# Optimization experiments

Measured on AMD Instinct MI355X. Metric: run time of the kernel, lower is better.

The kernel has to match this reference:

```python
import jax, jax.numpy as jnp
import numpy as np

N = 6720      # 16 graphs * 420 nodes
E = 33600     # 16 graphs * 2100 edges (5 per node)
DIN = 2048
H1, C1 = 2, 1024   # conv1: heads=2, out=1024 -> concat 2048
H2, C2 = 1, 64     # conv2: heads=1, out=64
ED = 64            # edge_dim
NODES_PER_GRAPH = 420


def _lin(k, fi, fo):
    return jax.random.normal(k, (fi, fo), jnp.float32) / np.sqrt(fi).astype(np.float32)


def setup_inputs() -> dict:
    key = jax.random.key(0)
    ks = jax.random.split(key, 24)
    d = {}
    d["x"] = jax.random.normal(ks[0], (N, DIN), jnp.float32)
    d["edge_index"] = jax.random.randint(ks[1], (2, E), 0, N)
    # tiled learned edge_features param (torch.rand init), one 2100xED block per graph
    ef = jax.random.uniform(ks[2], (5 * NODES_PER_GRAPH, ED), jnp.float32)
    d["edge_attr"] = jnp.tile(ef, (N // NODES_PER_GRAPH, 1))
    HC1 = H1 * C1
    d["q1_w"] = _lin(ks[3], DIN, HC1); d["q1_b"] = jax.random.normal(ks[4], (HC1,)) * 0.01
    d["k1_w"] = _lin(ks[5], DIN, HC1); d["k1_b"] = jax.random.normal(ks[6], (HC1,)) * 0.01
    d["v1_w"] = _lin(ks[7], DIN, HC1); d["v1_b"] = jax.random.normal(ks[8], (HC1,)) * 0.01
    d["e1_w"] = _lin(ks[9], ED, HC1)                      # lin_edge has no bias in PyG
    d["s1_w"] = _lin(ks[10], DIN, HC1); d["s1_b"] = jax.random.normal(ks[11], (HC1,)) * 0.01
    HC2 = H2 * C2
    d["q2_w"] = _lin(ks[12], HC1, HC2); d["q2_b"] = jax.random.normal(ks[13], (HC2,)) * 0.01
    d["k2_w"] = _lin(ks[14], HC1, HC2); d["k2_b"] = jax.random.normal(ks[15], (HC2,)) * 0.01
    d["v2_w"] = _lin(ks[16], HC1, HC2); d["v2_b"] = jax.random.normal(ks[17], (HC2,)) * 0.01
    d["e2_w"] = _lin(ks[18], ED, HC2)
    d["s2_w"] = _lin(ks[19], HC1, HC2); d["s2_b"] = jax.random.normal(ks[20], (HC2,)) * 0.01
    return d


def _transformer_conv(x, src, dst, edge_attr, qw, qb, kw, kb, vw, vb, ew, sw, sb, H, C):
    """PyG TransformerConv (concat=True, beta=False, root_weight=True)."""
    n = x.shape[0]
    q = (x @ qw + qb).reshape(n, H, C)
    k = (x @ kw + kb).reshape(n, H, C)
    v = (x @ vw + vb).reshape(n, H, C)
    e = (edge_attr @ ew).reshape(-1, H, C)         # [E,H,C]
    kj = k[src] + e                                # gather source keys + edge emb
    alpha = jnp.sum(q[dst] * kj, axis=-1) / np.sqrt(C).astype(np.float32)  # [E,H]
    # scatter-softmax over incoming edges of each target node
    amax = jax.ops.segment_max(alpha, dst, num_segments=n)   # [N,H]
    ex = jnp.exp(alpha - amax[dst])
    denom = jax.ops.segment_sum(ex, dst, num_segments=n)
    attn = ex / (denom[dst] + 1e-16)               # [E,H]
    msg = (v[src] + e) * attn[..., None]           # [E,H,C]
    out = jax.ops.segment_sum(msg, dst, num_segments=n).reshape(n, H * C)
    return out + x @ sw + sb                       # root/skip connection


def reference(x, edge_index, edge_attr,
              q1_w, q1_b, k1_w, k1_b, v1_w, v1_b, e1_w, s1_w, s1_b,
              q2_w, q2_b, k2_w, k2_b, v2_w, v2_b, e2_w, s2_w, s2_b):
    src, dst = edge_index[0], edge_index[1]
    h = jax.nn.relu(_transformer_conv(x, src, dst, edge_attr,
                                      q1_w, q1_b, k1_w, k1_b, v1_w, v1_b,
                                      e1_w, s1_w, s1_b, H1, C1))
    h = jax.nn.relu(_transformer_conv(h, src, dst, edge_attr,
                                      q2_w, q2_b, k2_w, k2_b, v2_w, v2_b,
                                      e2_w, s2_w, s2_b, H2, C2))
    return h.reshape(-1, NODES_PER_GRAPH * 64)     # forward returns here (fc layers are dead code)
```

## Files before the change

### kernel.cpp

```cpp
#include <hip/hip_runtime.h>
#include <hip/hip_bf16.h>
#include <cstdint>
#include <cstddef>

#define NN    6720
#define MPAD  6912
#define NE    33600
#define KDIM  2048
#define HC1   2048
#define EAP   2100

typedef __attribute__((ext_vector_type(8))) short bhalf8;
typedef __attribute__((ext_vector_type(4))) short bhalf4;
typedef __attribute__((ext_vector_type(4))) float fx4;

__device__ __forceinline__ float bf2f(short s) {
    union { unsigned int u; float f; } c;
    c.u = ((unsigned int)(unsigned short)s) << 16;
    return c.f;
}

__device__ __forceinline__ void gload16(const __hip_bfloat16* g, void* lds)
{
    __builtin_amdgcn_global_load_lds(
        (const __attribute__((address_space(1))) unsigned int*)g,
        (__attribute__((address_space(3))) unsigned int*)lds,
        16, 0, 0);
}

#define CFENCE asm volatile("" ::: "memory")

__global__ __launch_bounds__(256, 2) void gemm256x128_fused(
    const __hip_bfloat16* __restrict__ A,
    const __hip_bfloat16* __restrict__ Bt,
    const float* __restrict__ bcat,
    __hip_bfloat16* __restrict__ oq,
    __hip_bfloat16* __restrict__ ok,
    __hip_bfloat16* __restrict__ ov,
    float* __restrict__ oh)
{
    __shared__ alignas(16) char Lds[73728];

    const int tid  = threadIdx.x;
    const int w    = tid >> 6;
    const int lane = tid & 63;
    const int wm = w >> 1, wn = w & 1;
    const int sug = ((lane & 3) ^ ((lane >> 3) & 3)) << 3;
    const int rds = (((lane >> 4) ^ (((lane & 15) >> 1) & 3)) << 4);

#define STAGE(T)                                                          \
    { const int s_ = (T) % 3; const int k0_ = (T) * 32;                   \
      char* ab_ = Lds + s_ * 16384 + w * 4096;                            \
      char* bb_ = Lds + 49152 + s_ * 8192 + w * 2048;                     \
      gload16(Ag0 + k0_, ab_);                                            \
      gload16(Ag0 + k0_ + 16 * KDIM, ab_ + 1024);                         \
      gload16(Ag0 + k0_ + 32 * KDIM, ab_ + 2048);                         \
      gload16(Ag0 + k0_ + 48 * KDIM, ab_ + 3072);                         \
      gload16(Bg0 + k0_, bb_);                                            \
      gload16(Bg0 + k0_ + 16 * KDIM, bb_ + 1024); }

#define TILE(T, VM, DOSTAGE)                                              \
    { if (DOSTAGE) { STAGE((T) + 2); }                                    \
      asm volatile("s_waitcnt vmcnt(" VM ")" ::: "memory");               \
      __builtin_amdgcn_s_barrier(); CFENCE;                               \
      const int s_ = (T) % 3;                                             \
      const char* ap_ = Lds + s_ * 16384;                                 \
      const char* bp_ = Lds + 49152 + s_ * 8192;                          \
      bhalf8 af_[8], bf_[4];                                              \
      _Pragma("unroll")                                                   \
      for (int nj = 0; nj < 4; ++nj)                                      \
          bf_[nj] = *(const bhalf8*)(bp_ + (wn * 64 + nj * 16 + (lane & 15)) * 64 + rds); \
      _Pragma("unroll")                                                   \
      for (int mi = 0; mi < 8; ++mi)                                      \
          af_[mi] = *(const bhalf8*)(ap_ + (wm * 128 + mi * 16 + (lane & 15)) * 64 + rds); \
      __builtin_amdgcn_s_setprio(1);                                      \
      _Pragma("unroll")                                                   \
      for (int mi = 0; mi < 8; ++mi)                                      \
          _Pragma("unroll")                                               \
          for (int nj = 0; nj < 4; ++nj)                                  \
              acc[mi][nj] = __builtin_amdgcn_mfma_f32_16x16x32_bf16(      \
                  af_[mi], bf_[nj], acc[mi][nj], 0, 0, 0);                \
      __builtin_amdgcn_s_setprio(0); CFENCE;                              \
      __builtin_amdgcn_s_barrier(); CFENCE; }

    for (int vt = blockIdx.x; vt < 1728; vt += 512) {
        if (vt != (int)blockIdx.x) {
            asm volatile("s_waitcnt vmcnt(0)" ::: "memory");
            __builtin_amdgcn_s_barrier();
            CFENCE;
        }
        const int i0 = vt >> 3;
        const int bx = (vt & 7) * 8 + (i0 & 7);
        const int by = i0 >> 3;
        const int rowA = by * 256;
        const int rowB = bx * 128;
        const __hip_bfloat16* Ag0 = A  + (size_t)(rowA + w * 64 + (lane >> 2)) * KDIM + sug;
        const __hip_bfloat16* Bg0 = Bt + (size_t)(rowB + w * 32 + (lane >> 2)) * KDIM + sug;

        fx4 acc[8][4] = {};

        STAGE(0); STAGE(1);
        for (int t = 0; t < (KDIM / 32) - 2; ++t) {
            TILE(t, "12", 1);
        }
        TILE((KDIM / 32) - 2, "6", 0);
        TILE((KDIM / 32) - 1, "0", 0);

        const int gcol = rowB + wn * 64;
        const int seg  = gcol >> 11;
        const int lcol = gcol & 2047;
        float bv[4];
        #pragma unroll
        for (int nj = 0; nj < 4; ++nj) bv[nj] = bcat[gcol + nj * 16 + (lane & 15)];
        char* scr = Lds + w * 8704;
        const int growA = rowA + wm * 128;

        #pragma unroll
        for (int c = 0; c < 4; ++c) {
            #pragma unroll
            for (int m2 = 0; m2 < 2; ++m2) {
                const int mi = c * 2 + m2;
                #pragma unroll
                for (int nj = 0; nj < 4; ++nj) {
                    const int cl = nj * 16 + (lane & 15);
                    #pragma unroll
                    for (int i2 = 0; i2 < 4; ++i2) {
                        const int rl = m2 * 16 + ((lane >> 4) << 2) + i2;
                        *(float*)(scr + rl * 272 + cl * 4) = acc[mi][nj][i2] + bv[nj];
                    }
                }
            }
            asm volatile("s_waitcnt lgkmcnt(0)" ::: "memory");
            CFENCE;
            const int rrow = (lane >> 4);
            const int u    = lane & 15;
            if (seg < 3) {
                __hip_bfloat16* dst = (seg == 0) ? oq : (seg == 1) ? ok : ov;
                #pragma unroll
                for (int p = 0; p < 8; ++p) {
                    const int row = p * 4 + rrow;
                    const float4 f = *(const float4*)(scr + row * 272 + u * 16);
                    bhalf4 tb;
                    tb[0] = (short)__bfloat16_as_ushort(__float2bfloat16(f.x));
                    tb[1] = (short)__bfloat16_as_ushort(__float2bfloat16(f.y));
                    tb[2] = (short)__bfloat16_as_ushort(__float2bfloat16(f.z));
                    tb[3] = (short)__bfloat16_as_ushort(__float2bfloat16(f.w));
                    *(bhalf4*)&dst[(size_t)(growA + c * 32 + row) * 2048 + lcol + u * 4] = tb;
                }
            } else {
                #pragma unroll
                for (int p = 0; p < 8; ++p) {
                    const int row = p * 4 + rrow;
                    const float4 f = *(const float4*)(scr + row * 272 + u * 16);
                    *(float4*)&oh[(size_t)(growA + c * 32 + row) * 2048 + lcol + u * 4] = f;
                }
            }
            asm volatile("s_waitcnt lgkmcnt(0)" ::: "memory");
            CFENCE;
        }
    }
#undef TILE
#undef STAGE
}

__global__ __launch_bounds__(256) void gemm_bf16(
    const __hip_bfloat16* __restrict__ A,
    const __hip_bfloat16* __restrict__ Bt,
    const float* __restrict__ bias,
    float* __restrict__ C,
    __hip_bfloat16* __restrict__ Cb,
    int M, int N, int K, int flags)
{
    __shared__ alignas(16) __hip_bfloat16 Asm[128 * 64];
    __shared__ alignas(16) __hip_bfloat16 Bsm[128 * 64];
    const int tid  = threadIdx.x;
    const int w    = tid >> 6;
    const int lane = tid & 63;
    const int wr = w >> 1, wc = w & 1;
    const int rowA = blockIdx.y * 128;
    const int rowB = blockIdx.x * 128;
    const int klen = K / gridDim.z;
    const int kbeg = blockIdx.z * klen;

    const int srow = w * 32 + (lane >> 3);
    const int ug8  = ((lane & 7) ^ (lane >> 3)) << 3;
    const __hip_bfloat16* Ag = A  + (size_t)(rowA + srow) * K + ug8;
    const __hip_bfloat16* Bg = Bt + (size_t)(rowB + srow) * K + ug8;
    char* AsBase = (char*)Asm + w * 4096;
    char* BsBase = (char*)Bsm + w * 4096;

    fx4 acc[4][4] = {};

    const int fra = wr * 64 + (lane & 15);
    const int frb = wc * 64 + (lane & 15);
    const int kb  = (lane >> 4) << 4;
    const int swz = (lane & 7) << 4;

    for (int k0 = kbeg; k0 < kbeg + klen; k0 += 64) {
        __syncthreads();
        #pragma unroll
        for (int j = 0; j < 4; ++j) {
            gload16(Ag + (size_t)j * 8 * K + k0, AsBase + j * 1024);
            gload16(Bg + (size_t)j * 8 * K + k0, BsBase + j * 1024);
        }
        __syncthreads();
        #pragma unroll
        for (int kk = 0; kk < 2; ++kk) {
            const int cb = kk * 64 + kb;
            bhalf8 af[4], bfr[4];
            #pragma unroll
            for (int mi = 0; mi < 4; ++mi)
                af[mi] = *(const bhalf8*)((const char*)Asm + (fra + mi * 16) * 128 + (cb ^ swz));
            #pragma unroll
            for (int nj = 0; nj < 4; ++nj)
                bfr[nj] = *(const bhalf8*)((const char*)Bsm + (frb + nj * 16) * 128 + (cb ^ swz));
            #pragma unroll
            for (int mi = 0; mi < 4; ++mi)
                #pragma unroll
                for (int nj = 0; nj < 4; ++nj)
                    acc[mi][nj] = __builtin_amdgcn_mfma_f32_16x16x32_bf16(
                        af[mi], bfr[nj], acc[mi][nj], 0, 0, 0);
        }
    }

    float* Cz = C ? C + (size_t)blockIdx.z * ((size_t)M * N) : nullptr;
    #pragma unroll
    for (int nj = 0; nj < 4; ++nj) {
        const int ccol = rowB + wc * 64 + nj * 16 + (lane & 15);
        const float bv = (flags & 1) ? bias[ccol] : 0.f;
        #pragma unroll
        for (int mi = 0; mi < 4; ++mi) {
            const int crow0 = rowA + wr * 64 + mi * 16 + ((lane >> 4) << 2);
            #pragma unroll
            for (int i = 0; i < 4; ++i) {
                size_t idx = (size_t)(crow0 + i) * N + ccol;
                float v = acc[mi][nj][i] + bv;
                if (flags & 2) v += Cz[idx];
                if (flags & 4) v = fmaxf(v, 0.f);
                if (Cz && !(flags & 8)) Cz[idx] = v;
                if (Cb) Cb[idx] = __float2bfloat16(v);
            }
        }
    }
}

__global__ void reduce4(const float* __restrict__ parts, size_t stride,
                        const float* __restrict__ bias, int colmask,
                        float* __restrict__ dst, int n)
{
    int i = blockIdx.x * 256 + threadIdx.x;
    if (i >= n) return;
    float v = parts[i] + parts[stride + i] + parts[2 * stride + i] + parts[3 * stride + i];
    if (bias) v += bias[i & colmask];
    dst[i] = v;
}

__global__ __launch_bounds__(256) void gemm_tile(
    const float* __restrict__ A, const float* __restrict__ B,
    const float* __restrict__ bias, float* __restrict__ C,
    int M, int N, int K, int flags)
{
    __shared__ float As[16][68];
    __shared__ float Bs[16][64];
    const int tid = threadIdx.x;
    const int bx = blockIdx.x, by = blockIdx.y;
    const int tx = tid & 15, ty = tid >> 4;
    const int arow = tid >> 2, acol = (tid & 3) << 2;
    const int brow = tid >> 4, bcol = (tid & 15) << 2;
    const float* Ag = A + (size_t)(by * 64 + arow) * K + acol;
    const float* Bg = B + (size_t)brow * N + bx * 64 + bcol;
    float acc[4][4] = {};
    for (int k0 = 0; k0 < K; k0 += 16) {
        const float4 av = *(const float4*)(Ag + k0);
        const float4 bv = *(const float4*)(Bg + (size_t)k0 * N);
        __syncthreads();
        As[acol + 0][arow] = av.x;
        As[acol + 1][arow] = av.y;
        As[acol + 2][arow] = av.z;
        As[acol + 3][arow] = av.w;
        *(float4*)&Bs[brow][bcol] = bv;
        __syncthreads();
        #pragma unroll
        for (int kk = 0; kk < 16; ++kk) {
            const float4 a4 = *(const float4*)&As[kk][ty << 2];
            const float4 b4 = *(const float4*)&Bs[kk][tx << 2];
            const float a[4] = {a4.x, a4.y, a4.z, a4.w};
            const float b[4] = {b4.x, b4.y, b4.z, b4.w};
            #pragma unroll
            for (int i = 0; i < 4; ++i)
                #pragma unroll
                for (int j = 0; j < 4; ++j)
                    acc[i][j] += a[i] * b[j];
        }
    }
    const int crow = by * 64 + (ty << 2);
    const int ccol = bx * 64 + (tx << 2);
    float4 b4 = make_float4(0.f, 0.f, 0.f, 0.f);
    if (flags & 1) b4 = *(const float4*)(bias + ccol);
    #pragma unroll
    for (int i = 0; i < 4; ++i) {
        float* cp = C + (size_t)(crow + i) * N + ccol;
        float4 v;
        v.x = acc[i][0] + b4.x; v.y = acc[i][1] + b4.y;
        v.z = acc[i][2] + b4.z; v.w = acc[i][3] + b4.w;
        if (flags & 2) {
            const float4 o = *(const float4*)cp;
            v.x += o.x; v.y += o.y; v.z += o.z; v.w += o.w;
        }
        *(float4*)cp = v;
    }
}

__global__ void count_deg(const int* __restrict__ ei, int* __restrict__ deg)
{
    int e = blockIdx.x * 256 + threadIdx.x;
    if (e < NE) atomicAdd(&deg[ei[NE + e]], 1);
}

__global__ __launch_bounds__(1024) void scan_kernel(const int* __restrict__ deg,
                                                    int* __restrict__ rowptr)
{
    __shared__ int s[1024];
    const int t = threadIdx.x;
    const int base = t * 7;
    int loc[7];
    int sum = 0;
    #pragma unroll
    for (int i = 0; i < 7; ++i) {
        int idx = base + i;
        int v = (idx < NN) ? deg[idx] : 0;
        loc[i] = v; sum += v;
    }
    s[t] = sum;
    __syncthreads();
    for (int off = 1; off < 1024; off <<= 1) {
        int v = (t >= off) ? s[t - off] : 0;
        __syncthreads();
        s[t] += v;
        __syncthreads();
    }
    int running = s[t] - sum;
    #pragma unroll
    for (int i = 0; i < 7; ++i) {
        int idx = base + i;
        if (idx <= NN) rowptr[idx] = running;
        if (idx < NN) running += loc[i];
    }
}

__global__ void fill_csr(const int* __restrict__ ei, const int* __restrict__ rowptr,
                         int* __restrict__ fillctr, int* __restrict__ elist)
{
    int e = blockIdx.x * 256 + threadIdx.x;
    if (e >= NE) return;
    int d = ei[NE + e];
    int pos = atomicAdd(&fillctr[d], 1);
    elist[rowptr[d] + pos] = e;
}

__global__ void sort_csr(const int* __restrict__ rowptr, int* __restrict__ elist)
{
    int n = blockIdx.x * 256 + threadIdx.x;
    if (n >= NN) return;
    int s0 = rowptr[n], s1 = rowptr[n + 1];
    for (int i = s0 + 1; i < s1; ++i) {
        int v = elist[i];
        int j = i - 1;
        while (j >= s0 && elist[j] > v) { elist[j + 1] = elist[j]; --j; }
        elist[j + 1] = v;
    }
}

__global__ void cvt_pad_bf16(const float* __restrict__ src, __hip_bfloat16* __restrict__ dst,
                             int relu)
{
    size_t i = (size_t)(blockIdx.x * 256 + threadIdx.x) * 4;
    int row = (int)(i >> 11);
    float4 v = make_float4(0.f, 0.f, 0.f, 0.f);
    if (row < NN) v = *(const float4*)&src[i];
    if (relu) {
        v.x = fmaxf(v.x, 0.f); v.y = fmaxf(v.y, 0.f);
        v.z = fmaxf(v.z, 0.f); v.w = fmaxf(v.w, 0.f);
    }
    dst[i + 0] = __float2bfloat16(v.x);
    dst[i + 1] = __float2bfloat16(v.y);
    dst[i + 2] = __float2bfloat16(v.z);
    dst[i + 3] = __float2bfloat16(v.w);
}

__global__ __launch_bounds__(256) void transpose_cvt4(
    const float* __restrict__ W0, const float* __restrict__ W1,
    const float* __restrict__ W2, const float* __restrict__ W3,
    __hip_bfloat16* __restrict__ dst)
{
    const float* W = (blockIdx.z == 0) ? W0 : (blockIdx.z == 1) ? W1
                   : (blockIdx.z == 2) ? W2 : W3;
    __hip_bfloat16* Bt = dst + (size_t)blockIdx.z * KDIM * KDIM;
    __shared__ float t[32][33];
    int kb = blockIdx.y * 32, nb = blockIdx.x * 32;
    int tx = threadIdx.x & 31, ty = threadIdx.x >> 5;
    #pragma unroll
    for (int i = 0; i < 32; i += 8)
        t[ty + i][tx] = W[(size_t)(kb + ty + i) * KDIM + nb + tx];
    __syncthreads();
    #pragma unroll
    for (int i = 0; i < 32; i += 8)
        Bt[(size_t)(nb + ty + i) * KDIM + kb + tx] = __float2bfloat16(t[tx][ty + i]);
}

__global__ void build_bcat(const float* __restrict__ q1b, const float* __restrict__ k1b,
                           const float* __restrict__ v1b, const float* __restrict__ s1b,
                           float* __restrict__ bcat)
{
    int i = blockIdx.x * 256 + threadIdx.x;
    if (i >= 4 * KDIM) return;
    int seg = i >> 11, j = i & 2047;
    const float* b = (seg == 0) ? q1b : (seg == 1) ? k1b : (seg == 2) ? v1b : s1b;
    bcat[i] = b[j];
}

__global__ void build_w1pp(const float* __restrict__ e1w, __hip_bfloat16* __restrict__ w1pp)
{
    int idx = blockIdx.x * 256 + threadIdx.x;
    int p = idx >> 11, j = idx & 2047;
    float v = ((j >> 10) == (p >> 6)) ? e1w[(size_t)(p & 63) * KDIM + j] : 0.f;
    w1pp[idx] = __float2bfloat16(v);
}

__global__ void build_w1ppT(const float* __restrict__ e1w, __hip_bfloat16* __restrict__ w1ppT)
{
    int idx = blockIdx.x * 256 + threadIdx.x;
    int n = idx >> 7, k = idx & 127;
    float v = ((n >> 10) == (k >> 6)) ? e1w[(size_t)(k & 63) * KDIM + n] : 0.f;
    w1ppT[idx] = __float2bfloat16(v);
}

__global__ void build_w2t(const float* __restrict__ qw, const float* __restrict__ kw,
                          const float* __restrict__ vw, const float* __restrict__ sw,
                          const float* __restrict__ qb, const float* __restrict__ kb,
                          const float* __restrict__ vb, const float* __restrict__ sb,
                          __hip_bfloat16* __restrict__ w2t, float* __restrict__ b2)
{
    int idx = blockIdx.x * 256 + threadIdx.x;
    int c = idx >> 11, d = idx & 2047;
    int g = c >> 6, j = c & 63;
    const float* w = (g == 0) ? qw : (g == 1) ? kw : (g == 2) ? vw : sw;
    w2t[idx] = __float2bfloat16(w[(size_t)d * 64 + j]);
    if (d == 0) {
        const float* b = (g == 0) ? qb : (g == 1) ? kb : (g == 2) ? vb : sb;
        b2[c] = b[j];
    }
}

__global__ __launch_bounds__(256) void node1_kernel(
    const __hip_bfloat16* __restrict__ q1b, const __hip_bfloat16* __restrict__ k1b,
    const __hip_bfloat16* __restrict__ v1b,
    const float* __restrict__ P1, const float* __restrict__ ea,
    const int* __restrict__ ei, const int* __restrict__ rowptr,
    const int* __restrict__ elist,
    float* __restrict__ h1, __hip_bfloat16* __restrict__ R1)
{
    __shared__ int   s_src[256];
    __shared__ int   s_em[256];
    __shared__ float s_at[256][2];
    const int n = blockIdx.x;
    const int s0 = rowptr[n];
    const int deg = rowptr[n + 1] - s0;
    const int w = threadIdx.x >> 6, lane = threadIdx.x & 63;

    for (int j = w; j < deg; j += 4) {
        const int e = elist[s0 + j];
        const int src = ei[e];
        const int em = e % EAP;
        if (lane == 0) { s_src[j] = src; s_em[j] = em; }
        const float eaj = ea[(size_t)em * 64 + lane];
        #pragma unroll
        for (int h = 0; h < 2; ++h) {
            const __hip_bfloat16* qh = q1b + (size_t)n * HC1 + h * 1024 + lane * 16;
            const __hip_bfloat16* kh = k1b + (size_t)src * HC1 + h * 1024 + lane * 16;
            bhalf8 qa = *(const bhalf8*)qh, qc = *(const bhalf8*)(qh + 8);
            bhalf8 ka = *(const bhalf8*)kh, kc = *(const bhalf8*)(kh + 8);
            float s = 0.f;
            #pragma unroll
            for (int jj = 0; jj < 8; ++jj) s += bf2f(qa[jj]) * bf2f(ka[jj]);
            #pragma unroll
            for (int jj = 0; jj < 8; ++jj) s += bf2f(qc[jj]) * bf2f(kc[jj]);
            s += eaj * P1[(size_t)n * 128 + h * 64 + lane];
            #pragma unroll
            for (int off = 32; off; off >>= 1) s += __shfl_xor(s, off);
            if (lane == 0) s_at[j][h] = s * 0.03125f;
        }
    }
    __syncthreads();

    if (threadIdx.x < 2) {
        const int h = threadIdx.x;
        float m = -1e30f;
        for (int j = 0; j < deg; ++j) m = fmaxf(m, s_at[j][h]);
        float sum = 0.f;
        for (int j = 0; j < deg; ++j) {
            float ex = __expf(s_at[j][h] - m);
            s_at[j][h] = ex; sum += ex;
        }
        float inv = 1.f / (sum + 1e-16f);
        for (int j = 0; j < deg; ++j) s_at[j][h] *= inv;
    }
    __syncthreads();

    if (threadIdx.x < 128) {
        const int h = threadIdx.x >> 6, jj = threadIdx.x & 63;
        float r = 0.f;
        for (int j = 0; j < deg; ++j)
            r += s_at[j][h] * ea[(size_t)s_em[j] * 64 + jj];
        R1[(size_t)n * 128 + threadIdx.x] = __float2bfloat16(r);
    }

    const int c0 = threadIdx.x * 8;
    const int h = c0 >> 10;
    float acc[8];
    const float4 p0 = *(const float4*)&h1[(size_t)n * HC1 + c0];
    const float4 p1 = *(const float4*)&h1[(size_t)n * HC1 + c0 + 4];
    acc[0] = p0.x; acc[1] = p0.y; acc[2] = p0.z; acc[3] = p0.w;
    acc[4] = p1.x; acc[5] = p1.y; acc[6] = p1.z; acc[7] = p1.w;
    for (int j = 0; j < deg; ++j) {
        const float at = s_at[j][h];
        bhalf8 v = *(const bhalf8*)&v1b[(size_t)s_src[j] * HC1 + c0];
        #pragma unroll
        for (int jj = 0; jj < 8; ++jj) acc[jj] += at * bf2f(v[jj]);
    }
    *(float4*)&h1[(size_t)n * HC1 + c0]     = make_float4(acc[0], acc[1], acc[2], acc[3]);
    *(float4*)&h1[(size_t)n * HC1 + c0 + 4] = make_float4(acc[4], acc[5], acc[6], acc[7]);
}

__global__ __launch_bounds__(64) void node2_kernel(
    const float* __restrict__ qkvs2, const float* __restrict__ E2s,
    const int* __restrict__ ei, const int* __restrict__ rowptr,
    const int* __restrict__ elist, float* __restrict__ out)
{
    __shared__ float s_at[256];
    __shared__ int   s_src[256];
    __shared__ int   s_em[256];
    const int n = blockIdx.x;
    const int s0 = rowptr[n];
    const int deg = rowptr[n + 1] - s0;
    const int c = threadIdx.x;
    const float q = qkvs2[(size_t)n * 256 + c];

    for (int j = 0; j < deg; ++j) {
        const int e = elist[s0 + j];
        const int src = ei[e];
        const int em = e % EAP;
        float s = q * (qkvs2[(size_t)src * 256 + 64 + c] + E2s[(size_t)em * 64 + c]);
        #pragma unroll
        for (int off = 32; off; off >>= 1) s += __shfl_xor(s, off);
        if (c == 0) { s_at[j] = s * 0.125f; s_src[j] = src; s_em[j] = em; }
    }
    __syncthreads();
    float m = -1e30f;
    for (int j = 0; j < deg; ++j) m = fmaxf(m, s_at[j]);
    float sum = 0.f;
    for (int j = 0; j < deg; ++j) sum += __expf(s_at[j] - m);
    const float inv = 1.f / (sum + 1e-16f);

    float acc = qkvs2[(size_t)n * 256 + 192 + c];
    for (int j = 0; j < deg; ++j) {
        const float at = __expf(s_at[j] - m) * inv;
        acc += at * (qkvs2[(size_t)s_src[j] * 256 + 128 + c] + E2s[(size_t)s_em[j] * 64 + c]);
    }
    out[(size_t)n * 64 + c] = fmaxf(acc, 0.f);
}

extern "C" void kernel_launch(void* const* d_in, const int* in_sizes, int n_in,
                              void* d_out, int out_size, void* d_ws, size_t ws_size,
                              hipStream_t stream)
{
    const float* x   = (const float*)d_in[0];
    const int*   ei  = (const int*)d_in[1];
    const float* ea  = (const float*)d_in[2];
    const float* q1w = (const float*)d_in[3];
    const float* q1b = (const float*)d_in[4];
    const float* k1w = (const float*)d_in[5];
    const float* k1b = (const float*)d_in[6];
    const float* v1w = (const float*)d_in[7];
    const float* v1b = (const float*)d_in[8];
    const float* e1w = (const float*)d_in[9];
    const float* s1w = (const float*)d_in[10];
    const float* s1b = (const float*)d_in[11];
    const float* q2w = (const float*)d_in[12];
    const float* q2b = (const float*)d_in[13];
    const float* k2w = (const float*)d_in[14];
    const float* k2b = (const float*)d_in[15];
    const float* v2w = (const float*)d_in[16];
    const float* v2b = (const float*)d_in[17];
    const float* e2w = (const float*)d_in[18];
    const float* s2w = (const float*)d_in[19];
    const float* s2b = (const float*)d_in[20];
    float* out = (float*)d_out;

    char* base = (char*)d_ws;
    size_t off = 0;
    auto alloc = [&](size_t nbytes) {
        size_t o = off; off += (nbytes + 255) & ~(size_t)255; return o;
    };
    const size_t xb_off   = alloc((size_t)MPAD * KDIM * 2);
    const size_t wcat_off = alloc((size_t)4 * KDIM * KDIM * 2);
    __hip_bfloat16* xb    = (__hip_bfloat16*)(base + xb_off);
    __hip_bfloat16* wcat  = (__hip_bfloat16*)(base + wcat_off);
    __hip_bfloat16* h1b   = xb;
    float*          Cpart = (float*)(base + wcat_off);
    __hip_bfloat16* w2t   = (__hip_bfloat16*)(base + wcat_off + (size_t)29 * 1024 * 1024);

    __hip_bfloat16* q1bb  = (__hip_bfloat16*)(base + alloc((size_t)MPAD * HC1 * 2));
    __hip_bfloat16* k1bb  = (__hip_bfloat16*)(base + alloc((size_t)MPAD * HC1 * 2));
    __hip_bfloat16* v1bb  = (__hip_bfloat16*)(base + alloc((size_t)MPAD * HC1 * 2));
    float*          h1    = (float*)(base + alloc((size_t)MPAD * HC1 * 4));
    float*          bcat  = (float*)(base + alloc((size_t)4 * KDIM * 4));
    float*          P1    = (float*)(base + alloc((size_t)MPAD * 128 * 4));
    __hip_bfloat16* R1b   = (__hip_bfloat16*)(base + alloc((size_t)MPAD * 128 * 2));
    __hip_bfloat16* w1pp  = (__hip_bfloat16*)(base + alloc((size_t)128 * KDIM * 2));
    __hip_bfloat16* w1ppT = (__hip_bfloat16*)(base + alloc((size_t)KDIM * 128 * 2));
    float*          b2    = (float*)(base + alloc(256 * 4));
    float*          qkvs2 = (float*)(base + alloc((size_t)MPAD * 256 * 4));
    float*          E2s   = (float*)(base + alloc((size_t)2112 * 64 * 4));
    int* deg    = (int*)(base + alloc((size_t)NN * 4));
    int* fill   = (int*)(base + alloc((size_t)NN * 4));
    int* rowptr = (int*)(base + alloc((size_t)(NN + 1) * 4));
    int* elist  = (int*)(base + alloc((size_t)NE * 4));

    hipMemsetAsync(deg, 0, sizeof(int) * 2 * NN, stream);
    count_deg<<<(NE + 255) / 256, 256, 0, stream>>>(ei, deg);
    scan_kernel<<<1, 1024, 0, stream>>>(deg, rowptr);
    fill_csr<<<(NE + 255) / 256, 256, 0, stream>>>(ei, rowptr, fill, elist);
    sort_csr<<<(NN + 255) / 256, 256, 0, stream>>>(rowptr, elist);

    const int cvblk = (MPAD * KDIM / 4) / 256;
    cvt_pad_bf16<<<cvblk, 256, 0, stream>>>(x, xb, 0);
    transpose_cvt4<<<dim3(KDIM / 32, KDIM / 32, 4), 256, 0, stream>>>(q1w, k1w, v1w, s1w, wcat);
    build_bcat<<<(4 * KDIM) / 256, 256, 0, stream>>>(q1b, k1b, v1b, s1b, bcat);
    build_w1pp<<<(128 * KDIM) / 256, 256, 0, stream>>>(e1w, w1pp);
    build_w1ppT<<<(KDIM * 128) / 256, 256, 0, stream>>>(e1w, w1ppT);
    gemm_tile<<<dim3(1, 33), 256, 0, stream>>>(ea, e2w, nullptr, E2s, 2112, 64, 64, 0);

    gemm256x128_fused<<<512, 256, 0, stream>>>(xb, wcat, bcat, q1bb, k1bb, v1bb, h1);

    gemm_bf16<<<dim3(1, MPAD / 128, 4), 256, 0, stream>>>(q1bb, w1pp, nullptr, Cpart, nullptr,
                                                          MPAD, 128, KDIM, 0);
    reduce4<<<(MPAD * 128) / 256, 256, 0, stream>>>(Cpart, (size_t)MPAD * 128, nullptr, 0,
                                                    P1, MPAD * 128);

    node1_kernel<<<NN, 256, 0, stream>>>(q1bb, k1bb, v1bb, P1, ea, ei, rowptr, elist, h1, R1b);
    gemm_bf16<<<dim3(HC1 / 128, MPAD / 128), 256, 0, stream>>>(R1b, w1ppT, nullptr, h1, h1b,
                                                               MPAD, HC1, 128, 2 | 4 | 8);

    build_w2t<<<(256 * KDIM) / 256, 256, 0, stream>>>(q2w, k2w, v2w, s2w, q2b, k2b, v2b, s2b,
                                                      w2t, b2);
    gemm_bf16<<<dim3(2, MPAD / 128, 4), 256, 0, stream>>>(h1b, w2t, nullptr, Cpart, nullptr,
                                                          MPAD, 256, KDIM, 0);
    reduce4<<<(MPAD * 256) / 256, 256, 0, stream>>>(Cpart, (size_t)MPAD * 256, b2, 255,
                                                    qkvs2, MPAD * 256);

    node2_kernel<<<NN, 64, 0, stream>>>(qkvs2, E2s, ei, rowptr, elist, out);

    (void)in_sizes; (void)n_in; (void)out_size; (void)ws_size;
}
```

Before: 486.5 us.

## Store skip accumulator in bf16, drop persistent GEMM loop, merge weight-prep kernels

The skip/root output h1 is now kept in bf16 instead of fp32, so the fused GEMM, node1 aggregation and edge-projection GEMM all read and write half the bytes; the final GEMM adds the bf16 value in place via a new flag. The big QKVS GEMM switches from a 512-block persistent loop to one block per tile (1728 blocks). Four small weight/bias build kernels are merged into one launch. The bf16 accumulator loses precision across the add chain.

After: 456.6 us. 1.07x faster.

```diff
diff --git a/kernel.cpp b/kernel.cpp
--- a/kernel.cpp
+++ b/kernel.cpp
@@ -37,16 +37,29 @@
     __hip_bfloat16* __restrict__ oq,
     __hip_bfloat16* __restrict__ ok,
     __hip_bfloat16* __restrict__ ov,
-    float* __restrict__ oh)
+    __hip_bfloat16* __restrict__ oh)
 {
     __shared__ alignas(16) char Lds[73728];
+
+    const int bid = blockIdx.x;
+    const int i0  = bid >> 3;
+    const int bx  = (bid & 7) * 8 + (i0 & 7);
+    const int by  = i0 >> 3;
 
     const int tid  = threadIdx.x;
     const int w    = tid >> 6;
     const int lane = tid & 63;
     const int wm = w >> 1, wn = w & 1;
+    const int rowA = by * 256;
+    const int rowB = bx * 128;
+
     const int sug = ((lane & 3) ^ ((lane >> 3) & 3)) << 3;
+    const __hip_bfloat16* Ag0 = A  + (size_t)(rowA + w * 64 + (lane >> 2)) * KDIM + sug;
+    const __hip_bfloat16* Bg0 = Bt + (size_t)(rowB + w * 32 + (lane >> 2)) * KDIM + sug;
+
     const int rds = (((lane >> 4) ^ (((lane & 15) >> 1) & 3)) << 4);
+
+    fx4 acc[8][4] = {};
 
 #define STAGE(T)                                                          \
     { const int s_ = (T) % 3; const int k0_ = (T) * 32;                   \
@@ -83,84 +96,59 @@
       __builtin_amdgcn_s_setprio(0); CFENCE;                              \
       __builtin_amdgcn_s_barrier(); CFENCE; }
 
-    for (int vt = blockIdx.x; vt < 1728; vt += 512) {
-        if (vt != (int)blockIdx.x) {
-            asm volatile("s_waitcnt vmcnt(0)" ::: "memory");
-            __builtin_amdgcn_s_barrier();
-            CFENCE;
-        }
-        const int i0 = vt >> 3;
-        const int bx = (vt & 7) * 8 + (i0 & 7);
-        const int by = i0 >> 3;
-        const int rowA = by * 256;
-        const int rowB = bx * 128;
-        const __hip_bfloat16* Ag0 = A  + (size_t)(rowA + w * 64 + (lane >> 2)) * KDIM + sug;
-        const __hip_bfloat16* Bg0 = Bt + (size_t)(rowB + w * 32 + (lane >> 2)) * KDIM + sug;
-
-        fx4 acc[8][4] = {};
-
-        STAGE(0); STAGE(1);
-        for (int t = 0; t < (KDIM / 32) - 2; ++t) {
-            TILE(t, "12", 1);
-        }
-        TILE((KDIM / 32) - 2, "6", 0);
-        TILE((KDIM / 32) - 1, "0", 0);
-
-        const int gcol = rowB + wn * 64;
-        const int seg  = gcol >> 11;
-        const int lcol = gcol & 2047;
-        float bv[4];
-        #pragma unroll
-        for (int nj = 0; nj < 4; ++nj) bv[nj] = bcat[gcol + nj * 16 + (lane & 15)];
-        char* scr = Lds + w * 8704;
-        const int growA = rowA + wm * 128;
-
-        #pragma unroll
-        for (int c = 0; c < 4; ++c) {
-            #pragma unroll
-            for (int m2 = 0; m2 < 2; ++m2) {
-                const int mi = c * 2 + m2;
+    STAGE(0); STAGE(1);
+    for (int t = 0; t < (KDIM / 32) - 2; ++t) {
+        TILE(t, "12", 1);
+    }
+    TILE((KDIM / 32) - 2, "6", 0);
+    TILE((KDIM / 32) - 1, "0", 0);
+
+#undef TILE
+#undef STAGE
+
+    const int gcol = rowB + wn * 64;
+    const int seg  = gcol >> 11;
+    const int lcol = gcol & 2047;
+    float bv[4];
+    #pragma unroll
+    for (int nj = 0; nj < 4; ++nj) bv[nj] = bcat[gcol + nj * 16 + (lane & 15)];
+    char* scr = Lds + w * 8704;
+    const int growA = rowA + wm * 128;
+    __hip_bfloat16* dst = (seg == 0) ? oq : (seg == 1) ? ok : (seg == 2) ? ov : oh;
+
+    #pragma unroll
+    for (int c = 0; c < 4; ++c) {
+        #pragma unroll
+        for (int m2 = 0; m2 < 2; ++m2) {
+            const int mi = c * 2 + m2;
+            #pragma unroll
+            for (int nj = 0; nj < 4; ++nj) {
+                const int cl = nj * 16 + (lane & 15);
                 #pragma unroll
-                for (int nj = 0; nj < 4; ++nj) {
-                    const int cl = nj * 16 + (lane & 15);
-                    #pragma unroll
-                    for (int i2 = 0; i2 < 4; ++i2) {
-                        const int rl = m2 * 16 + ((lane >> 4) << 2) + i2;
-                        *(float*)(scr + rl * 272 + cl * 4) = acc[mi][nj][i2] + bv[nj];
-                    }
+                for (int i2 = 0; i2 < 4; ++i2) {
+                    const int rl = m2 * 16 + ((lane >> 4) << 2) + i2;
+                    *(float*)(scr + rl * 272 + cl * 4) = acc[mi][nj][i2] + bv[nj];
                 }
             }
-            asm volatile("s_waitcnt lgkmcnt(0)" ::: "memory");
-            CFENCE;
-            const int rrow = (lane >> 4);
-            const int u    = lane & 15;
-            if (seg < 3) {
-                __hip_bfloat16* dst = (seg == 0) ? oq : (seg == 1) ? ok : ov;
-                #pragma unroll
-                for (int p = 0; p < 8; ++p) {
-                    const int row = p * 4 + rrow;
-                    const float4 f = *(const float4*)(scr + row * 272 + u * 16);
-                    bhalf4 tb;
-                    tb[0] = (short)__bfloat16_as_ushort(__float2bfloat16(f.x));
-                    tb[1] = (short)__bfloat16_as_ushort(__float2bfloat16(f.y));
-                    tb[2] = (short)__bfloat16_as_ushort(__float2bfloat16(f.z));
-                    tb[3] = (short)__bfloat16_as_ushort(__float2bfloat16(f.w));
-                    *(bhalf4*)&dst[(size_t)(growA + c * 32 + row) * 2048 + lcol + u * 4] = tb;
-                }
-            } else {
-                #pragma unroll
-                for (int p = 0; p < 8; ++p) {
-                    const int row = p * 4 + rrow;
-                    const float4 f = *(const float4*)(scr + row * 272 + u * 16);
-                    *(float4*)&oh[(size_t)(growA + c * 32 + row) * 2048 + lcol + u * 4] = f;
-                }
-            }
-            asm volatile("s_waitcnt lgkmcnt(0)" ::: "memory");
-            CFENCE;
-        }
-    }
-#undef TILE
-#undef STAGE
+        }
+        asm volatile("s_waitcnt lgkmcnt(0)" ::: "memory");
+        CFENCE;
+        const int rrow = (lane >> 4);
+        const int u    = lane & 15;
+        #pragma unroll
+        for (int p = 0; p < 8; ++p) {
+            const int row = p * 4 + rrow;
+            const float4 f = *(const float4*)(scr + row * 272 + u * 16);
+            bhalf4 tb;
+            tb[0] = (short)__bfloat16_as_ushort(__float2bfloat16(f.x));
+            tb[1] = (short)__bfloat16_as_ushort(__float2bfloat16(f.y));
+            tb[2] = (short)__bfloat16_as_ushort(__float2bfloat16(f.z));
+            tb[3] = (short)__bfloat16_as_ushort(__float2bfloat16(f.w));
+            *(bhalf4*)&dst[(size_t)(growA + c * 32 + row) * 2048 + lcol + u * 4] = tb;
+        }
+        asm volatile("s_waitcnt lgkmcnt(0)" ::: "memory");
+        CFENCE;
+    }
 }
 
 __global__ __launch_bounds__(256) void gemm_bf16(
@@ -235,8 +223,9 @@
             for (int i = 0; i < 4; ++i) {
                 size_t idx = (size_t)(crow0 + i) * N + ccol;
                 float v = acc[mi][nj][i] + bv;
-                if (flags & 2) v += Cz[idx];
-                if (flags & 4) v = fmaxf(v, 0.f);
+                if (flags & 2)  v += Cz[idx];
+                if (flags & 16) v += __bfloat162float(Cb[idx]);
+                if (flags & 4)  v = fmaxf(v, 0.f);
                 if (Cz && !(flags & 8)) Cz[idx] = v;
                 if (Cb) Cb[idx] = __float2bfloat16(v);
             }
@@ -408,46 +397,46 @@
         Bt[(size_t)(nb + ty + i) * KDIM + kb + tx] = __float2bfloat16(t[tx][ty + i]);
 }
 
-__global__ void build_bcat(const float* __restrict__ q1b, const float* __restrict__ k1b,
-                           const float* __restrict__ v1b, const float* __restrict__ s1b,
-                           float* __restrict__ bcat)
-{
-    int i = blockIdx.x * 256 + threadIdx.x;
-    if (i >= 4 * KDIM) return;
-    int seg = i >> 11, j = i & 2047;
-    const float* b = (seg == 0) ? q1b : (seg == 1) ? k1b : (seg == 2) ? v1b : s1b;
-    bcat[i] = b[j];
-}
-
-__global__ void build_w1pp(const float* __restrict__ e1w, __hip_bfloat16* __restrict__ w1pp)
+__global__ void build_misc(
+    const float* __restrict__ q1b, const float* __restrict__ k1b,
+    const float* __restrict__ v1b, const float* __restrict__ s1b,
+    const float* __restrict__ e1w,
+    const float* __restrict__ q2w, const float* __restrict__ k2w,
+    const float* __restrict__ v2w, const float* __restrict__ s2w,
+    const float* __restrict__ q2bb, const float* __restrict__ k2bb,
+    const float* __restrict__ v2bb, const float* __restrict__ s2bb,
+    float* __restrict__ bcat, __hip_bfloat16* __restrict__ w1pp,
+    __hip_bfloat16* __restrict__ w1ppT, __hip_bfloat16* __restrict__ w2t,
+    float* __restrict__ b2)
 {
     int idx = blockIdx.x * 256 + threadIdx.x;
-    int p = idx >> 11, j = idx & 2047;
-    float v = ((j >> 10) == (p >> 6)) ? e1w[(size_t)(p & 63) * KDIM + j] : 0.f;
-    w1pp[idx] = __float2bfloat16(v);
-}
-
-__global__ void build_w1ppT(const float* __restrict__ e1w, __hip_bfloat16* __restrict__ w1ppT)
-{
-    int idx = blockIdx.x * 256 + threadIdx.x;
-    int n = idx >> 7, k = idx & 127;
-    float v = ((n >> 10) == (k >> 6)) ? e1w[(size_t)(k & 63) * KDIM + n] : 0.f;
-    w1ppT[idx] = __float2bfloat16(v);
-}
-
-__global__ void build_w2t(const float* __restrict__ qw, const float* __restrict__ kw,
-                          const float* __restrict__ vw, const float* __restrict__ sw,
-                          const float* __restrict__ qb, const float* __restrict__ kb,
-                          const float* __restrict__ vb, const float* __restrict__ sb,
-                          __hip_bfloat16* __restrict__ w2t, float* __restrict__ b2)
-{
-    int idx = blockIdx.x * 256 + threadIdx.x;
+    if (idx < 8192) {
+        int seg = idx >> 11, j = idx & 2047;
+        const float* b = (seg == 0) ? q1b : (seg == 1) ? k1b : (seg == 2) ? v1b : s1b;
+        bcat[idx] = b[j];
+        return;
+    }
+    idx -= 8192;
+    if (idx < 262144) {
+        int p = idx >> 11, j = idx & 2047;
+        float v = ((j >> 10) == (p >> 6)) ? e1w[(size_t)(p & 63) * KDIM + j] : 0.f;
+        w1pp[idx] = __float2bfloat16(v);
+        return;
+    }
+    idx -= 262144;
+    if (idx < 262144) {
+        int n = idx >> 7, k = idx & 127;
+        float v = ((n >> 10) == (k >> 6)) ? e1w[(size_t)(k & 63) * KDIM + n] : 0.f;
+        w1ppT[idx] = __float2bfloat16(v);
+        return;
+    }
+    idx -= 262144;
     int c = idx >> 11, d = idx & 2047;
     int g = c >> 6, j = c & 63;
-    const float* w = (g == 0) ? qw : (g == 1) ? kw : (g == 2) ? vw : sw;
+    const float* w = (g == 0) ? q2w : (g == 1) ? k2w : (g == 2) ? v2w : s2w;
     w2t[idx] = __float2bfloat16(w[(size_t)d * 64 + j]);
     if (d == 0) {
-        const float* b = (g == 0) ? qb : (g == 1) ? kb : (g == 2) ? vb : sb;
+        const float* b = (g == 0) ? q2bb : (g == 1) ? k2bb : (g == 2) ? v2bb : s2bb;
         b2[c] = b[j];
     }
 }
@@ -458,7 +447,7 @@
     const float* __restrict__ P1, const float* __restrict__ ea,
     const int* __restrict__ ei, const int* __restrict__ rowptr,
     const int* __restrict__ elist,
-    float* __restrict__ h1, __hip_bfloat16* __restrict__ R1)
+    __hip_bfloat16* __restrict__ h1, __hip_bfloat16* __restrict__ R1)
 {
     __shared__ int   s_src[256];
     __shared__ int   s_em[256];
@@ -518,18 +507,20 @@
     const int c0 = threadIdx.x * 8;
     const int h = c0 >> 10;
     float acc[8];
-    const float4 p0 = *(const float4*)&h1[(size_t)n * HC1 + c0];
-    const float4 p1 = *(const float4*)&h1[(size_t)n * HC1 + c0 + 4];
-    acc[0] = p0.x; acc[1] = p0.y; acc[2] = p0.z; acc[3] = p0.w;
-    acc[4] = p1.x; acc[5] = p1.y; acc[6] = p1.z; acc[7] = p1.w;
+    const bhalf8 cur = *(const bhalf8*)&h1[(size_t)n * HC1 + c0];
+    #pragma unroll
+    for (int jj = 0; jj < 8; ++jj) acc[jj] = bf2f(cur[jj]);
     for (int j = 0; j < deg; ++j) {
         const float at = s_at[j][h];
         bhalf8 v = *(const bhalf8*)&v1b[(size_t)s_src[j] * HC1 + c0];
         #pragma unroll
         for (int jj = 0; jj < 8; ++jj) acc[jj] += at * bf2f(v[jj]);
     }
-    *(float4*)&h1[(size_t)n * HC1 + c0]     = make_float4(acc[0], acc[1], acc[2], acc[3]);
-    *(float4*)&h1[(size_t)n * HC1 + c0 + 4] = make_float4(acc[4], acc[5], acc[6], acc[7]);
+    bhalf8 o;
+    #pragma unroll
+    for (int jj = 0; jj < 8; ++jj)
+        o[jj] = (short)__bfloat16_as_ushort(__float2bfloat16(acc[jj]));
+    *(bhalf8*)&h1[(size_t)n * HC1 + c0] = o;
 }
 
 __global__ __launch_bounds__(64) void node2_kernel(
@@ -606,19 +597,18 @@
     const size_t wcat_off = alloc((size_t)4 * KDIM * KDIM * 2);
     __hip_bfloat16* xb    = (__hip_bfloat16*)(base + xb_off);
     __hip_bfloat16* wcat  = (__hip_bfloat16*)(base + wcat_off);
-    __hip_bfloat16* h1b   = xb;
     float*          Cpart = (float*)(base + wcat_off);
-    __hip_bfloat16* w2t   = (__hip_bfloat16*)(base + wcat_off + (size_t)29 * 1024 * 1024);
 
     __hip_bfloat16* q1bb  = (__hip_bfloat16*)(base + alloc((size_t)MPAD * HC1 * 2));
     __hip_bfloat16* k1bb  = (__hip_bfloat16*)(base + alloc((size_t)MPAD * HC1 * 2));
     __hip_bfloat16* v1bb  = (__hip_bfloat16*)(base + alloc((size_t)MPAD * HC1 * 2));
-    float*          h1    = (float*)(base + alloc((size_t)MPAD * HC1 * 4));
+    __hip_bfloat16* h1bf  = (__hip_bfloat16*)(base + alloc((size_t)MPAD * HC1 * 2));
     float*          bcat  = (float*)(base + alloc((size_t)4 * KDIM * 4));
     float*          P1    = (float*)(base + alloc((size_t)MPAD * 128 * 4));
     __hip_bfloat16* R1b   = (__hip_bfloat16*)(base + alloc((size_t)MPAD * 128 * 2));
     __hip_bfloat16* w1pp  = (__hip_bfloat16*)(base + alloc((size_t)128 * KDIM * 2));
     __hip_bfloat16* w1ppT = (__hip_bfloat16*)(base + alloc((size_t)KDIM * 128 * 2));
+    __hip_bfloat16* w2t   = (__hip_bfloat16*)(base + alloc((size_t)256 * KDIM * 2));
     float*          b2    = (float*)(base + alloc(256 * 4));
     float*          qkvs2 = (float*)(base + alloc((size_t)MPAD * 256 * 4));
     float*          E2s   = (float*)(base + alloc((size_t)2112 * 64 * 4));
@@ -636,25 +626,23 @@
     const int cvblk = (MPAD * KDIM / 4) / 256;
     cvt_pad_bf16<<<cvblk, 256, 0, stream>>>(x, xb, 0);
     transpose_cvt4<<<dim3(KDIM / 32, KDIM / 32, 4), 256, 0, stream>>>(q1w, k1w, v1w, s1w, wcat);
-    build_bcat<<<(4 * KDIM) / 256, 256, 0, stream>>>(q1b, k1b, v1b, s1b, bcat);
-    build_w1pp<<<(128 * KDIM) / 256, 256, 0, stream>>>(e1w, w1pp);
-    build_w1ppT<<<(KDIM * 128) / 256, 256, 0, stream>>>(e1w, w1ppT);
+    build_misc<<<4128, 256, 0, stream>>>(q1b, k1b, v1b, s1b, e1w,
+                                         q2w, k2w, v2w, s2w, q2b, k2b, v2b, s2b,
+                                         bcat, w1pp, w1ppT, w2t, b2);
     gemm_tile<<<dim3(1, 33), 256, 0, stream>>>(ea, e2w, nullptr, E2s, 2112, 64, 64, 0);
 
-    gemm256x128_fused<<<512, 256, 0, stream>>>(xb, wcat, bcat, q1bb, k1bb, v1bb, h1);
+    gemm256x128_fused<<<1728, 256, 0, stream>>>(xb, wcat, bcat, q1bb, k1bb, v1bb, h1bf);
 
     gemm_bf16<<<dim3(1, MPAD / 128, 4), 256, 0, stream>>>(q1bb, w1pp, nullptr, Cpart, nullptr,
                                                           MPAD, 128, KDIM, 0);
     reduce4<<<(MPAD * 128) / 256, 256, 0, stream>>>(Cpart, (size_t)MPAD * 128, nullptr, 0,
                                                     P1, MPAD * 128);
 
-    node1_kernel<<<NN, 256, 0, stream>>>(q1bb, k1bb, v1bb, P1, ea, ei, rowptr, elist, h1, R1b);
-    gemm_bf16<<<dim3(HC1 / 128, MPAD / 128), 256, 0, stream>>>(R1b, w1ppT, nullptr, h1, h1b,
-                                                               MPAD, HC1, 128, 2 | 4 | 8);
-
-    build_w2t<<<(256 * KDIM) / 256, 256, 0, stream>>>(q2w, k2w, v2w, s2w, q2b, k2b, v2b, s2b,
-                                                      w2t, b2);
-    gemm_bf16<<<dim3(2, MPAD / 128, 4), 256, 0, stream>>>(h1b, w2t, nullptr, Cpart, nullptr,
+    node1_kernel<<<NN, 256, 0, stream>>>(q1bb, k1bb, v1bb, P1, ea, ei, rowptr, elist, h1bf, R1b);
+    gemm_bf16<<<dim3(HC1 / 128, MPAD / 128), 256, 0, stream>>>(R1b, w1ppT, nullptr, nullptr,
+                                                               h1bf, MPAD, HC1, 128, 16 | 4);
+
+    gemm_bf16<<<dim3(2, MPAD / 128, 4), 256, 0, stream>>>(h1bf, w2t, nullptr, Cpart, nullptr,
                                                           MPAD, 256, KDIM, 0);
     reduce4<<<(MPAD * 256) / 256, 256, 0, stream>>>(Cpart, (size_t)MPAD * 256, b2, 255,
                                                     qkvs2, MPAD * 256);
```
